# Kernel tuning notes

Hardware: AMD Instinct MI355X
Metric: run time of the kernel (lower is better)

Reference implementation:

```python
import jax, jax.numpy as jnp
import numpy as np

PAD = 4
MAX_DISP = 4


def setup_inputs() -> dict:
    key = jax.random.key(0)
    k1, k2 = jax.random.split(key)
    in1 = jax.random.normal(k1, (8, 256, 128, 128), dtype=jnp.float32)
    in2 = jax.random.normal(k2, (8, 256, 128, 128), dtype=jnp.float32)
    return {"in1": in1, "in2": in2}


def reference(in1, in2):
    # in1, in2: [B, C, H, W]
    H, W = in1.shape[2], in1.shape[3]
    in2_pad = jnp.pad(in2, ((0, 0), (0, 0), (PAD, PAD), (PAD, PAD)))
    D = 2 * MAX_DISP + 1  # 9 displacements per axis -> 81 output channels
    outs = []
    # torch.meshgrid('ij') + zip(offsetx, offsety): dy is the outer (slow) index,
    # dx the inner (fast) index.
    for dy in range(D):
        for dx in range(D):
            # mean over channel dim of elementwise product with shifted window
            corr = jnp.mean(in1 * in2_pad[:, :, dy:dy + H, dx:dx + W],
                            axis=1, keepdims=True)  # [B,1,H,W]
            outs.append(corr)
    return jnp.concatenate(outs, axis=1)  # [B, D*D, H, W]
```

## Files before the change

### kernel.cpp

```cpp
#include <hip/hip_runtime.h>


#define B_   8
#define C_   256
#define H_   128
#define W_   128
#define ND   9
#define TY   16
#define TW   16
#define CS   (H_ * W_)
#define NST  16
#define SB2  9216
#define S1OFF 73728
#define FOFF  106496
#define FAOFF 143360
#define LDS_TOTAL 159744

typedef short v8s __attribute__((ext_vector_type(8)));
typedef float v4f __attribute__((ext_vector_type(4)));

__device__ __forceinline__ unsigned short f2bf(float f) {
    union { float f; unsigned u; } v; v.f = f;
    return (unsigned short)((v.u + 0x7FFFu + ((v.u >> 16) & 1u)) >> 16);
}

__device__ __forceinline__ void dma16(const float* g, void* lds) {
    __builtin_amdgcn_global_load_lds(
        (const __attribute__((address_space(1))) void*)g,
        (__attribute__((address_space(3))) void*)lds, 16, 0, 0);
}

#define FENCE()     asm volatile("" ::: "memory")
#define WAITK_BAR() do {                                                          \
        if (w < 4) asm volatile("s_waitcnt vmcnt(7)\n\ts_barrier" ::: "memory");  \
        else       asm volatile("s_waitcnt vmcnt(6)\n\ts_barrier" ::: "memory");  \
    } while (0)
#define WAITV0_BAR() asm volatile("s_waitcnt vmcnt(0)\n\ts_barrier" ::: "memory")
#define LGKM0_BAR()  asm volatile("s_waitcnt lgkmcnt(0)\n\ts_barrier" ::: "memory")
#define LGKM0()      asm volatile("s_waitcnt lgkmcnt(0)" ::: "memory")

__global__ __launch_bounds__(512, 2)
void corr_mfma_kernel(const float* __restrict__ in1,
                      const float* __restrict__ in2,
                      float* __restrict__ out) {
    extern __shared__ __align__(16) char ldsbase[];
    float* S2 = (float*)ldsbase;
    float* S1 = (float*)(ldsbase + S1OFF);
    short* F  = (short*)(ldsbase + FOFF);
    short* FA = (short*)(ldsbase + FAOFF);
    float* EP = (float*)ldsbase;

    const int tid  = threadIdx.x;
    const int lane = tid & 63;
    const int w    = tid >> 6;

    const int lin = blockIdx.x;
    const int b   = lin & 7;
    const int idx = lin >> 3;
    const int x0  = (idx & 7) * TW;
    const int y0  = (idx >> 3) * TY;

    const int i_px = lane & 15;
    const int kb   = lane >> 4;

    const float* dsrc[5];
    int ddst[5];
    #pragma unroll
    for (int t = 0; t < 5; ++t) {
        if (w >= 4 && t >= 4) { dsrc[t] = in2; ddst[t] = 0; continue; }
        const int q   = (w < 4) ? (w * 5 + t) : (20 + (w - 4) * 4 + t);
        const int g   = q * 64 + lane;
        const int ccl = g / 144;
        const int rem = g % 144;
        const int r   = rem / 6;
        const int jg  = rem % 6;
        int gy = y0 - 4 + r;
        int gx = x0 - 4 + jg * 4;
        gy = gy < 0 ? 0 : (gy > H_ - 1 ? H_ - 1 : gy);
        gx = gx < 0 ? 0 : (gx > W_ - 4 ? W_ - 4 : gx);
        dsrc[t] = in2 + ((long)(b * C_) + ccl) * CS + gy * W_ + gx;
        ddst[t] = q * 1024;
    }
    const float* d1src[2];
    int d1dst[2];
    #pragma unroll
    for (int t = 0; t < 2; ++t) {
        const int q   = w * 2 + t;
        const int g   = q * 64 + lane;
        const int ch  = g >> 6;
        const int rem = g & 63;
        const int r   = rem >> 2;
        const int xg  = rem & 3;
        d1src[t] = in1 + ((long)(b * C_) + ch) * CS + (y0 + r) * W_ + x0 + xg * 4;
        d1dst[t] = q * 1024;
    }

    int rem_i[3], kbl_i[3];
    bool cval[3];
    #pragma unroll
    for (int it = 0; it < 3; ++it) {
        const int s2  = (tid + it * 512) % 1152;
        kbl_i[it] = s2 / 576;
        rem_i[it] = s2 % 576;
        const int r = rem_i[it] / 24, j = rem_i[it] % 24;
        cval[it] = ((unsigned)(y0 - 4 + r) < (unsigned)H_) &&
                   ((unsigned)(x0 - 4 + j) < (unsigned)W_);
    }
    const int r1  = tid >> 5;
    const int px1 = (tid >> 1) & 15;
    const int kb1 = tid & 1;

    v4f acc0[2][ND];
    v4f acc1[2][5];
    #pragma unroll
    for (int rw = 0; rw < 2; ++rw) {
        #pragma unroll
        for (int d = 0; d < ND; ++d) acc0[rw][d] = (v4f)0.0f;
        #pragma unroll
        for (int p = 0; p < 5; ++p)  acc1[rw][p] = (v4f)0.0f;
    }

#define ISSUE_G(s_) do {                                                      \
        const long so = (long)(s_) * 16 * CS;                                 \
        char* sb2 = (char*)S2 + ((s_) & 1) * 36864;                           \
        _Pragma("unroll")                                                     \
        for (int t = 0; t < 5; ++t)                                           \
            if (w < 4 || t < 4) dma16(dsrc[t] + so, sb2 + ddst[t]);           \
        char* sb1 = (char*)S1 + ((s_) & 1) * 16384;                           \
        _Pragma("unroll")                                                     \
        for (int t = 0; t < 2; ++t) dma16(d1src[t] + so, sb1 + d1dst[t]);     \
        FENCE();                                                              \
    } while (0)

#define CONVERT(s_) do {                                                      \
        const float* sb2 = S2 + ((s_) & 1) * SB2;                             \
        _Pragma("unroll")                                                     \
        for (int it = 0; it < 3; ++it) {                                      \
            if (it < 2 || tid < 128) {                                        \
                v8s pk;                                                       \
                _Pragma("unroll")                                             \
                for (int e = 0; e < 8; ++e)                                   \
                    pk[e] = (short)f2bf(sb2[kbl_i[it] * 4608 + rem_i[it] + e * 576]); \
                if (!cval[it]) pk = (v8s)0;                                   \
                const int kb32 = ((s_) & 1) * 2 + kbl_i[it];                  \
                *(v8s*)&F[kb32 * 4608 + (rem_i[it] << 3)] = pk;               \
            }                                                                 \
        }                                                                     \
        const float* sb1 = S1 + ((s_) & 1) * 4096;                            \
        v8s pa;                                                               \
        _Pragma("unroll")                                                     \
        for (int e = 0; e < 8; ++e)                                           \
            pa[e] = (short)f2bf(sb1[(kb1 * 8 + e) * 256 + r1 * 16 + px1]);    \
        *(v8s*)&FA[r1 * 512 + px1 * 32 + ((s_) & 1) * 16 + kb1 * 8] = pa;     \
    } while (0)

    ISSUE_G(0);
    ISSUE_G(1);
    WAITK_BAR();
    CONVERT(0);
    LGKM0_BAR();

    #pragma unroll
    for (int s = 0; s < NST; ++s) {
        if (s + 2 < NST) ISSUE_G(s + 2);

        if (s & 1) {
            const v8s af0 = *(const v8s*)&FA[(2 * w + 0) * 512 + i_px * 32 + kb * 8];
            const v8s af1 = *(const v8s*)&FA[(2 * w + 1) * 512 + i_px * 32 + kb * 8];
            #pragma unroll
            for (int u = 0; u < 10; ++u) {
                const int rj = (2 * w + u) * 24 + i_px;
                const v8s f = *(const v8s*)&F[kb * 4608 + (rj << 3)];
                if (u < 9)
                    acc0[0][u] = __builtin_amdgcn_mfma_f32_16x16x32_bf16(
                        af0, f, acc0[0][u], 0, 0, 0);
                if (u > 0)
                    acc0[1][u - 1] = __builtin_amdgcn_mfma_f32_16x16x32_bf16(
                        af1, f, acc0[1][u - 1], 0, 0, 0);
            }
            const int hi = i_px >> 3, j1 = 16 + (i_px & 7);
            #pragma unroll
            for (int u = 0; u < 10; ++u) {
                int r = 2 * w + hi + u;
                if (r > 23) r = 23;
                const int rj = r * 24 + j1;
                const v8s f = *(const v8s*)&F[kb * 4608 + (rj << 3)];
                if ((u & 1) == 0)
                    acc1[0][u >> 1] = __builtin_amdgcn_mfma_f32_16x16x32_bf16(
                        af0, f, acc1[0][u >> 1], 0, 0, 0);
                else
                    acc1[1][u >> 1] = __builtin_amdgcn_mfma_f32_16x16x32_bf16(
                        af1, f, acc1[1][u >> 1], 0, 0, 0);
            }
        }

        if (s + 2 < NST)       { WAITK_BAR(); }
        else if (s == NST - 2) { WAITV0_BAR(); }

        if (s < NST - 1) {
            CONVERT(s + 1);
            LGKM0_BAR();
        }
    }

    float* epw = EP + w * 384;
    const int g4 = lane >> 4;
    #pragma unroll
    for (int rw = 0; rw < 2; ++rw) {
        const int orow = y0 + 2 * w + rw;
        #pragma unroll
        for (int dy = 0; dy < ND; ++dy) {
            #pragma unroll
            for (int q = 0; q < 4; ++q)
                epw[(g4 * 4 + q) * 24 + i_px] = acc0[rw][dy][q];
            if ((i_px >> 3) == (dy & 1)) {
                #pragma unroll
                for (int q = 0; q < 4; ++q)
                    epw[(g4 * 4 + q) * 24 + 16 + (i_px & 7)] = acc1[rw][dy >> 1][q];
            }
            LGKM0();
            #pragma unroll
            for (int rep = 0; rep < 3; ++rep) {
                const int dx = g4 + rep * 4;
                if (dx < 9) {
                    const float v = epw[i_px * 24 + i_px + dx] * (1.0f / 256.0f);
                    out[(((long)b * 81 + dy * 9 + dx) * H_ + orow) * W_ + x0 + i_px] = v;
                }
            }
            LGKM0();
        }
    }
#undef ISSUE_G
#undef CONVERT
}

extern "C" void kernel_launch(void* const* d_in, const int* in_sizes, int n_in,
                              void* d_out, int out_size, void* d_ws, size_t ws_size,
                              hipStream_t stream) {
    const float* in1 = (const float*)d_in[0];
    const float* in2 = (const float*)d_in[1];
    float* outp      = (float*)d_out;
    (void)hipFuncSetAttribute((const void*)corr_mfma_kernel,
                              hipFuncAttributeMaxDynamicSharedMemorySize,
                              LDS_TOTAL);
    corr_mfma_kernel<<<512, 512, LDS_TOTAL, stream>>>(in1, in2, outp);
}
```

Measured before the change: 90.26 us.

## Widen tile to 32 columns with 1024-thread blocks and register-loaded in1 fragments

Doubles the output tile width to 16x32 and runs 256 blocks of 1024 threads (16 waves, one row each), which cuts the redundant halo traffic for in2 per output pixel. in1 is no longer staged through LDS. Each lane loads its A-fragment straight from global memory into registers a chunk ahead and converts it to bf16 in place. The in2 pipeline now streams 8 channels per stage into a four-deep bf16 ring, and the MFMAs run once per 32 channels. The trade-off is one block per CU with fewer blocks in flight, a hand-tuned vmcnt schedule, and strided uncoalesced-ish in1 loads.

```diff
diff --git a/kernel.cpp b/kernel.cpp
--- a/kernel.cpp
+++ b/kernel.cpp
@@ -7,14 +7,11 @@
 #define W_   128
 #define ND   9
 #define TY   16
-#define TW   16
+#define TW   32
 #define CS   (H_ * W_)
-#define NST  16
-#define SB2  9216
-#define S1OFF 73728
-#define FOFF  106496
-#define FAOFF 143360
-#define LDS_TOTAL 159744
+#define SB2F 7680
+#define FOFFB 61440
+#define LDS_TOTAL 122880
 
 typedef short v8s __attribute__((ext_vector_type(8)));
 typedef float v4f __attribute__((ext_vector_type(4)));
@@ -30,24 +27,26 @@
         (__attribute__((address_space(3))) void*)lds, 16, 0, 0);
 }
 
-#define FENCE()     asm volatile("" ::: "memory")
+#define FENCE()      asm volatile("" ::: "memory")
 #define WAITK_BAR() do {                                                          \
-        if (w < 4) asm volatile("s_waitcnt vmcnt(7)\n\ts_barrier" ::: "memory");  \
-        else       asm volatile("s_waitcnt vmcnt(6)\n\ts_barrier" ::: "memory");  \
+        if (w < 14) asm volatile("s_waitcnt vmcnt(2)\n\ts_barrier" ::: "memory"); \
+        else        asm volatile("s_waitcnt vmcnt(1)\n\ts_barrier" ::: "memory"); \
+    } while (0)
+#define WAITKA_BAR() do {                                                          \
+        if (w < 14) asm volatile("s_waitcnt vmcnt(18)\n\ts_barrier" ::: "memory"); \
+        else        asm volatile("s_waitcnt vmcnt(17)\n\ts_barrier" ::: "memory"); \
     } while (0)
 #define WAITV0_BAR() asm volatile("s_waitcnt vmcnt(0)\n\ts_barrier" ::: "memory")
 #define LGKM0_BAR()  asm volatile("s_waitcnt lgkmcnt(0)\n\ts_barrier" ::: "memory")
 #define LGKM0()      asm volatile("s_waitcnt lgkmcnt(0)" ::: "memory")
 
-__global__ __launch_bounds__(512, 2)
+__global__ __launch_bounds__(1024, 1)
 void corr_mfma_kernel(const float* __restrict__ in1,
                       const float* __restrict__ in2,
                       float* __restrict__ out) {
     extern __shared__ __align__(16) char ldsbase[];
     float* S2 = (float*)ldsbase;
-    float* S1 = (float*)(ldsbase + S1OFF);
-    short* F  = (short*)(ldsbase + FOFF);
-    short* FA = (short*)(ldsbase + FAOFF);
+    short* F  = (short*)(ldsbase + FOFFB);
     float* EP = (float*)ldsbase;
 
     const int tid  = threadIdx.x;
@@ -57,166 +56,151 @@
     const int lin = blockIdx.x;
     const int b   = lin & 7;
     const int idx = lin >> 3;
-    const int x0  = (idx & 7) * TW;
-    const int y0  = (idx >> 3) * TY;
+    const int x0  = (idx & 3) * TW;
+    const int y0  = (idx >> 2) * TY;
 
     const int i_px = lane & 15;
     const int kb   = lane >> 4;
 
-    const float* dsrc[5];
-    int ddst[5];
+    const float* dsrc[2];
+    int ddst[2];
     #pragma unroll
-    for (int t = 0; t < 5; ++t) {
-        if (w >= 4 && t >= 4) { dsrc[t] = in2; ddst[t] = 0; continue; }
-        const int q   = (w < 4) ? (w * 5 + t) : (20 + (w - 4) * 4 + t);
+    for (int t = 0; t < 2; ++t) {
+        if (t == 1 && w >= 14) { dsrc[t] = in2; ddst[t] = 0; continue; }
+        const int q   = (w < 14) ? (w * 2 + t) : (28 + (w - 14));
         const int g   = q * 64 + lane;
-        const int ccl = g / 144;
-        const int rem = g % 144;
-        const int r   = rem / 6;
-        const int jg  = rem % 6;
+        const int ch  = g / 240;
+        const int rem = g % 240;
+        const int r   = rem / 10;
+        const int jg  = rem % 10;
         int gy = y0 - 4 + r;
         int gx = x0 - 4 + jg * 4;
         gy = gy < 0 ? 0 : (gy > H_ - 1 ? H_ - 1 : gy);
         gx = gx < 0 ? 0 : (gx > W_ - 4 ? W_ - 4 : gx);
-        dsrc[t] = in2 + ((long)(b * C_) + ccl) * CS + gy * W_ + gx;
+        dsrc[t] = in2 + ((long)(b * C_) + ch) * CS + gy * W_ + gx;
         ddst[t] = q * 1024;
     }
-    const float* d1src[2];
-    int d1dst[2];
-    #pragma unroll
-    for (int t = 0; t < 2; ++t) {
-        const int q   = w * 2 + t;
-        const int g   = q * 64 + lane;
-        const int ch  = g >> 6;
-        const int rem = g & 63;
-        const int r   = rem >> 2;
-        const int xg  = rem & 3;
-        d1src[t] = in1 + ((long)(b * C_) + ch) * CS + (y0 + r) * W_ + x0 + xg * 4;
-        d1dst[t] = q * 1024;
-    }
-
-    int rem_i[3], kbl_i[3];
-    bool cval[3];
-    #pragma unroll
-    for (int it = 0; it < 3; ++it) {
-        const int s2  = (tid + it * 512) % 1152;
-        kbl_i[it] = s2 / 576;
-        rem_i[it] = s2 % 576;
-        const int r = rem_i[it] / 24, j = rem_i[it] % 24;
-        cval[it] = ((unsigned)(y0 - 4 + r) < (unsigned)H_) &&
-                   ((unsigned)(x0 - 4 + j) < (unsigned)W_);
-    }
-    const int r1  = tid >> 5;
-    const int px1 = (tid >> 1) & 15;
-    const int kb1 = tid & 1;
+
+    const float* pA =
+        in1 + ((long)b * C_ + kb * 8) * CS + (long)(y0 + w) * W_ + x0 + i_px;
+
+    const bool cact = (w < 15);
+    const int  crr  = tid / 40, cjj = tid % 40;
+    const bool cval = cact && ((unsigned)(y0 - 4 + crr) < (unsigned)H_) &&
+                              ((unsigned)(x0 - 4 + cjj) < (unsigned)W_);
 
     v4f acc0[2][ND];
     v4f acc1[2][5];
     #pragma unroll
-    for (int rw = 0; rw < 2; ++rw) {
+    for (int t = 0; t < 2; ++t) {
         #pragma unroll
-        for (int d = 0; d < ND; ++d) acc0[rw][d] = (v4f)0.0f;
+        for (int d = 0; d < ND; ++d) acc0[t][d] = (v4f)0.0f;
         #pragma unroll
-        for (int p = 0; p < 5; ++p)  acc1[rw][p] = (v4f)0.0f;
+        for (int p = 0; p < 5; ++p)  acc1[t][p] = (v4f)0.0f;
     }
+    float bufA[16], bufB[16];
+    v8s afA[2], afB[2];
 
 #define ISSUE_G(s_) do {                                                      \
-        const long so = (long)(s_) * 16 * CS;                                 \
-        char* sb2 = (char*)S2 + ((s_) & 1) * 36864;                           \
+        const long so = (long)(s_) * 8 * CS;                                  \
+        char* dst = (char*)S2 + ((s_) & 1) * 30720;                           \
+        dma16(dsrc[0] + so, dst + ddst[0]);                                   \
+        if (w < 14) dma16(dsrc[1] + so, dst + ddst[1]);                       \
+        FENCE();                                                              \
+    } while (0)
+
+#define ISSUE_A(cn_, buf_) do {                                               \
         _Pragma("unroll")                                                     \
-        for (int t = 0; t < 5; ++t)                                           \
-            if (w < 4 || t < 4) dma16(dsrc[t] + so, sb2 + ddst[t]);           \
-        char* sb1 = (char*)S1 + ((s_) & 1) * 16384;                           \
+        for (int t = 0; t < 2; ++t)                                           \
+            _Pragma("unroll")                                                 \
+            for (int e = 0; e < 8; ++e)                                       \
+                buf_[t * 8 + e] = pA[((long)(cn_) * 32 + e) * CS + t * 16];   \
+        FENCE();                                                              \
+    } while (0)
+
+#define AFRAG(buf_, af_) do {                                                 \
         _Pragma("unroll")                                                     \
-        for (int t = 0; t < 2; ++t) dma16(d1src[t] + so, sb1 + d1dst[t]);     \
-        FENCE();                                                              \
+        for (int t = 0; t < 2; ++t)                                           \
+            _Pragma("unroll")                                                 \
+            for (int e = 0; e < 8; ++e)                                       \
+                af_[t][e] = (short)f2bf(buf_[t * 8 + e]);                     \
     } while (0)
 
 #define CONVERT(s_) do {                                                      \
-        const float* sb2 = S2 + ((s_) & 1) * SB2;                             \
+        if (cact) {                                                           \
+            const float* sh = S2 + ((s_) & 1) * SB2F;                         \
+            v8s pk;                                                           \
+            _Pragma("unroll")                                                 \
+            for (int e = 0; e < 8; ++e)                                       \
+                pk[e] = (short)f2bf(sh[e * 960 + tid]);                       \
+            if (!cval) pk = (v8s)0;                                           \
+            *(v8s*)&F[(((s_) % 4) * 960 + tid) * 8] = pk;                     \
+        }                                                                     \
+    } while (0)
+
+#define MFMA_C(af_) do {                                                      \
         _Pragma("unroll")                                                     \
-        for (int it = 0; it < 3; ++it) {                                      \
-            if (it < 2 || tid < 128) {                                        \
-                v8s pk;                                                       \
-                _Pragma("unroll")                                             \
-                for (int e = 0; e < 8; ++e)                                   \
-                    pk[e] = (short)f2bf(sb2[kbl_i[it] * 4608 + rem_i[it] + e * 576]); \
-                if (!cval[it]) pk = (v8s)0;                                   \
-                const int kb32 = ((s_) & 1) * 2 + kbl_i[it];                  \
-                *(v8s*)&F[kb32 * 4608 + (rem_i[it] << 3)] = pk;               \
+        for (int t = 0; t < 2; ++t) {                                         \
+            _Pragma("unroll")                                                 \
+            for (int dy = 0; dy < ND; ++dy) {                                 \
+                const v8s f = *(const v8s*)&F[(kb * 960 + (w + dy) * 40 + t * 16 + i_px) * 8]; \
+                acc0[t][dy] = __builtin_amdgcn_mfma_f32_16x16x32_bf16(        \
+                    af_[t], f, acc0[t][dy], 0, 0, 0);                         \
+            }                                                                 \
+            const int hi = i_px >> 3, j1 = t * 16 + 16 + (i_px & 7);          \
+            _Pragma("unroll")                                                 \
+            for (int P = 0; P < 5; ++P) {                                     \
+                int r = w + 2 * P + hi;                                       \
+                if (r > 23) r = 23;            \
+                const v8s f = *(const v8s*)&F[(kb * 960 + r * 40 + j1) * 8];  \
+                acc1[t][P] = __builtin_amdgcn_mfma_f32_16x16x32_bf16(         \
+                    af_[t], f, acc1[t][P], 0, 0, 0);                          \
             }                                                                 \
         }                                                                     \
-        const float* sb1 = S1 + ((s_) & 1) * 4096;                            \
-        v8s pa;                                                               \
-        _Pragma("unroll")                                                     \
-        for (int e = 0; e < 8; ++e)                                           \
-            pa[e] = (short)f2bf(sb1[(kb1 * 8 + e) * 256 + r1 * 16 + px1]);    \
-        *(v8s*)&FA[r1 * 512 + px1 * 32 + ((s_) & 1) * 16 + kb1 * 8] = pa;     \
-    } while (0)
-
+    } while (0)
+
+#define CHUNK(c_, afc_, afn_, bufn_) do {                                     \
+        ISSUE_G(4*(c_)+2); WAITK_BAR();  CONVERT(4*(c_)+1); LGKM0_BAR();      \
+        ISSUE_G(4*(c_)+3); WAITK_BAR();  CONVERT(4*(c_)+2); LGKM0_BAR();      \
+        ISSUE_A((c_)+1, bufn_);                                               \
+        ISSUE_G(4*(c_)+4); WAITKA_BAR(); CONVERT(4*(c_)+3); LGKM0_BAR();      \
+        ISSUE_G(4*(c_)+5); MFMA_C(afc_); WAITK_BAR();                         \
+        CONVERT(4*(c_)+4); AFRAG(bufn_, afn_); LGKM0_BAR();                   \
+    } while (0)
+
+    ISSUE_A(0, bufA);
     ISSUE_G(0);
     ISSUE_G(1);
     WAITK_BAR();
+    AFRAG(bufA, afA);
     CONVERT(0);
     LGKM0_BAR();
 
-    #pragma unroll
-    for (int s = 0; s < NST; ++s) {
-        if (s + 2 < NST) ISSUE_G(s + 2);
-
-        if (s & 1) {
-            const v8s af0 = *(const v8s*)&FA[(2 * w + 0) * 512 + i_px * 32 + kb * 8];
-            const v8s af1 = *(const v8s*)&FA[(2 * w + 1) * 512 + i_px * 32 + kb * 8];
-            #pragma unroll
-            for (int u = 0; u < 10; ++u) {
-                const int rj = (2 * w + u) * 24 + i_px;
-                const v8s f = *(const v8s*)&F[kb * 4608 + (rj << 3)];
-                if (u < 9)
-                    acc0[0][u] = __builtin_amdgcn_mfma_f32_16x16x32_bf16(
-                        af0, f, acc0[0][u], 0, 0, 0);
-                if (u > 0)
-                    acc0[1][u - 1] = __builtin_amdgcn_mfma_f32_16x16x32_bf16(
-                        af1, f, acc0[1][u - 1], 0, 0, 0);
-            }
-            const int hi = i_px >> 3, j1 = 16 + (i_px & 7);
-            #pragma unroll
-            for (int u = 0; u < 10; ++u) {
-                int r = 2 * w + hi + u;
-                if (r > 23) r = 23;
-                const int rj = r * 24 + j1;
-                const v8s f = *(const v8s*)&F[kb * 4608 + (rj << 3)];
-                if ((u & 1) == 0)
-                    acc1[0][u >> 1] = __builtin_amdgcn_mfma_f32_16x16x32_bf16(
-                        af0, f, acc1[0][u >> 1], 0, 0, 0);
-                else
-                    acc1[1][u >> 1] = __builtin_amdgcn_mfma_f32_16x16x32_bf16(
-                        af1, f, acc1[1][u >> 1], 0, 0, 0);
-            }
-        }
-
-        if (s + 2 < NST)       { WAITK_BAR(); }
-        else if (s == NST - 2) { WAITV0_BAR(); }
-
-        if (s < NST - 1) {
-            CONVERT(s + 1);
-            LGKM0_BAR();
-        }
-    }
+    CHUNK(0, afA, afB, bufB);
+    CHUNK(1, afB, afA, bufA);
+    CHUNK(2, afA, afB, bufB);
+    CHUNK(3, afB, afA, bufA);
+    CHUNK(4, afA, afB, bufB);
+    CHUNK(5, afB, afA, bufA);
+    CHUNK(6, afA, afB, bufB);
+    ISSUE_G(30); WAITK_BAR();  CONVERT(29); LGKM0_BAR();
+    ISSUE_G(31); WAITK_BAR();  CONVERT(30); LGKM0_BAR();
+    WAITV0_BAR();              CONVERT(31); LGKM0_BAR();
+    MFMA_C(afB);
 
     float* epw = EP + w * 384;
     const int g4 = lane >> 4;
     #pragma unroll
-    for (int rw = 0; rw < 2; ++rw) {
-        const int orow = y0 + 2 * w + rw;
+    for (int t = 0; t < 2; ++t) {
         #pragma unroll
         for (int dy = 0; dy < ND; ++dy) {
             #pragma unroll
             for (int q = 0; q < 4; ++q)
-                epw[(g4 * 4 + q) * 24 + i_px] = acc0[rw][dy][q];
+                epw[(g4 * 4 + q) * 24 + i_px] = acc0[t][dy][q];
             if ((i_px >> 3) == (dy & 1)) {
                 #pragma unroll
                 for (int q = 0; q < 4; ++q)
-                    epw[(g4 * 4 + q) * 24 + 16 + (i_px & 7)] = acc1[rw][dy >> 1][q];
+                    epw[(g4 * 4 + q) * 24 + 16 + (i_px & 7)] = acc1[t][dy >> 1][q];
             }
             LGKM0();
             #pragma unroll
@@ -224,14 +208,18 @@
                 const int dx = g4 + rep * 4;
                 if (dx < 9) {
                     const float v = epw[i_px * 24 + i_px + dx] * (1.0f / 256.0f);
-                    out[(((long)b * 81 + dy * 9 + dx) * H_ + orow) * W_ + x0 + i_px] = v;
+                    out[(((long)b * 81 + dy * 9 + dx) * CS) + (y0 + w) * W_ + x0 + t * 16 + i_px] = v;
                 }
             }
             LGKM0();
         }
     }
 #undef ISSUE_G
+#undef ISSUE_A
+#undef AFRAG
 #undef CONVERT
+#undef MFMA_C
+#undef CHUNK
 }
 
 extern "C" void kernel_launch(void* const* d_in, const int* in_sizes, int n_in,
@@ -243,5 +231,5 @@
     (void)hipFuncSetAttribute((const void*)corr_mfma_kernel,
                               hipFuncAttributeMaxDynamicSharedMemorySize,
                               LDS_TOTAL);
-    corr_mfma_kernel<<<512, 512, LDS_TOTAL, stream>>>(in1, in2, outp);
-}
+    corr_mfma_kernel<<<256, 1024, LDS_TOTAL, stream>>>(in1, in2, outp);
+}
```

After: 258.2 us. +186.1%, slower.

## Double block size to 1024 threads with one output row per wave

Applied to the files above, without the earlier changes.

The kernel now launches 16 waves per block instead of 8, and each wave computes one output row instead of two. The in2/in1 DMA and conversion work is redistributed across the extra waves, and the vmcnt thresholds are adjusted to match the smaller per-wave load count. This halves the accumulator registers per thread and adds more waves to hide latency. In exchange it gives up reuse of the shared F fragments across two rows, which raises the total LDS fragment reads, and the 1024-thread barriers become more expensive.

```diff
diff --git a/kernel.cpp b/kernel.cpp
--- a/kernel.cpp
+++ b/kernel.cpp
@@ -32,14 +32,14 @@
 
 #define FENCE()     asm volatile("" ::: "memory")
 #define WAITK_BAR() do {                                                          \
-        if (w < 4) asm volatile("s_waitcnt vmcnt(7)\n\ts_barrier" ::: "memory");  \
-        else       asm volatile("s_waitcnt vmcnt(6)\n\ts_barrier" ::: "memory");  \
+        if (w < 4) asm volatile("s_waitcnt vmcnt(4)\n\ts_barrier" ::: "memory");  \
+        else       asm volatile("s_waitcnt vmcnt(3)\n\ts_barrier" ::: "memory");  \
     } while (0)
 #define WAITV0_BAR() asm volatile("s_waitcnt vmcnt(0)\n\ts_barrier" ::: "memory")
 #define LGKM0_BAR()  asm volatile("s_waitcnt lgkmcnt(0)\n\ts_barrier" ::: "memory")
 #define LGKM0()      asm volatile("s_waitcnt lgkmcnt(0)" ::: "memory")
 
-__global__ __launch_bounds__(512, 2)
+__global__ __launch_bounds__(1024, 4)
 void corr_mfma_kernel(const float* __restrict__ in1,
                       const float* __restrict__ in2,
                       float* __restrict__ out) {
@@ -63,12 +63,12 @@
     const int i_px = lane & 15;
     const int kb   = lane >> 4;
 
-    const float* dsrc[5];
-    int ddst[5];
-    #pragma unroll
-    for (int t = 0; t < 5; ++t) {
-        if (w >= 4 && t >= 4) { dsrc[t] = in2; ddst[t] = 0; continue; }
-        const int q   = (w < 4) ? (w * 5 + t) : (20 + (w - 4) * 4 + t);
+    const float* dsrc[3];
+    int ddst[3];
+    #pragma unroll
+    for (int t = 0; t < 3; ++t) {
+        if (w >= 4 && t >= 2) { dsrc[t] = in2; ddst[t] = 0; continue; }
+        const int q   = (w < 4) ? (w * 3 + t) : (12 + (w - 4) * 2 + t);
         const int g   = q * 64 + lane;
         const int ccl = g / 144;
         const int rem = g % 144;
@@ -81,62 +81,55 @@
         dsrc[t] = in2 + ((long)(b * C_) + ccl) * CS + gy * W_ + gx;
         ddst[t] = q * 1024;
     }
-    const float* d1src[2];
-    int d1dst[2];
-    #pragma unroll
-    for (int t = 0; t < 2; ++t) {
-        const int q   = w * 2 + t;
-        const int g   = q * 64 + lane;
+    const float* d1src;
+    int d1dst;
+    {
+        const int g   = w * 64 + lane;
         const int ch  = g >> 6;
         const int rem = g & 63;
         const int r   = rem >> 2;
         const int xg  = rem & 3;
-        d1src[t] = in1 + ((long)(b * C_) + ch) * CS + (y0 + r) * W_ + x0 + xg * 4;
-        d1dst[t] = q * 1024;
-    }
-
-    int rem_i[3], kbl_i[3];
-    bool cval[3];
-    #pragma unroll
-    for (int it = 0; it < 3; ++it) {
-        const int s2  = (tid + it * 512) % 1152;
+        d1src = in1 + ((long)(b * C_) + ch) * CS + (y0 + r) * W_ + x0 + xg * 4;
+        d1dst = w * 1024;
+    }
+
+    int rem_i[2], kbl_i[2];
+    bool cval[2];
+    #pragma unroll
+    for (int it = 0; it < 2; ++it) {
+        const int s2 = tid + it * 1024;
         kbl_i[it] = s2 / 576;
         rem_i[it] = s2 % 576;
         const int r = rem_i[it] / 24, j = rem_i[it] % 24;
         cval[it] = ((unsigned)(y0 - 4 + r) < (unsigned)H_) &&
                    ((unsigned)(x0 - 4 + j) < (unsigned)W_);
     }
-    const int r1  = tid >> 5;
+    const int r1  = (tid >> 5) & 15;
     const int px1 = (tid >> 1) & 15;
     const int kb1 = tid & 1;
 
-    v4f acc0[2][ND];
-    v4f acc1[2][5];
-    #pragma unroll
-    for (int rw = 0; rw < 2; ++rw) {
-        #pragma unroll
-        for (int d = 0; d < ND; ++d) acc0[rw][d] = (v4f)0.0f;
-        #pragma unroll
-        for (int p = 0; p < 5; ++p)  acc1[rw][p] = (v4f)0.0f;
-    }
+    v4f acc0[ND];
+    v4f acc1[5];
+    #pragma unroll
+    for (int d = 0; d < ND; ++d) acc0[d] = (v4f)0.0f;
+    #pragma unroll
+    for (int p = 0; p < 5; ++p)  acc1[p] = (v4f)0.0f;
 
 #define ISSUE_G(s_) do {                                                      \
         const long so = (long)(s_) * 16 * CS;                                 \
         char* sb2 = (char*)S2 + ((s_) & 1) * 36864;                           \
         _Pragma("unroll")                                                     \
-        for (int t = 0; t < 5; ++t)                                           \
-            if (w < 4 || t < 4) dma16(dsrc[t] + so, sb2 + ddst[t]);           \
-        char* sb1 = (char*)S1 + ((s_) & 1) * 16384;                           \
-        _Pragma("unroll")                                                     \
-        for (int t = 0; t < 2; ++t) dma16(d1src[t] + so, sb1 + d1dst[t]);     \
+        for (int t = 0; t < 3; ++t)                                           \
+            if (w < 4 || t < 2) dma16(dsrc[t] + so, sb2 + ddst[t]);           \
+        dma16(d1src + so, (char*)ldsbase + S1OFF + ((s_) & 1) * 16384 + d1dst); \
         FENCE();                                                              \
     } while (0)
 
 #define CONVERT(s_) do {                                                      \
         const float* sb2 = S2 + ((s_) & 1) * SB2;                             \
         _Pragma("unroll")                                                     \
-        for (int it = 0; it < 3; ++it) {                                      \
-            if (it < 2 || tid < 128) {                                        \
+        for (int it = 0; it < 2; ++it) {                                      \
+            if (it < 1 || tid < 128) {                                        \
                 v8s pk;                                                       \
                 _Pragma("unroll")                                             \
                 for (int e = 0; e < 8; ++e)                                   \
@@ -146,12 +139,14 @@
                 *(v8s*)&F[kb32 * 4608 + (rem_i[it] << 3)] = pk;               \
             }                                                                 \
         }                                                                     \
-        const float* sb1 = S1 + ((s_) & 1) * 4096;                            \
-        v8s pa;                                                               \
-        _Pragma("unroll")                                                     \
-        for (int e = 0; e < 8; ++e)                                           \
-            pa[e] = (short)f2bf(sb1[(kb1 * 8 + e) * 256 + r1 * 16 + px1]);    \
-        *(v8s*)&FA[r1 * 512 + px1 * 32 + ((s_) & 1) * 16 + kb1 * 8] = pa;     \
+        if (tid < 512) {                                                      \
+            const float* sb1 = S1 + ((s_) & 1) * 4096;                        \
+            v8s pa;                                                           \
+            _Pragma("unroll")                                                 \
+            for (int e = 0; e < 8; ++e)                                       \
+                pa[e] = (short)f2bf(sb1[(kb1 * 8 + e) * 256 + r1 * 16 + px1]); \
+            *(v8s*)&FA[r1 * 512 + px1 * 32 + ((s_) & 1) * 16 + kb1 * 8] = pa; \
+        }                                                                     \
     } while (0)
 
     ISSUE_G(0);
@@ -165,32 +160,23 @@
         if (s + 2 < NST) ISSUE_G(s + 2);
 
         if (s & 1) {
-            const v8s af0 = *(const v8s*)&FA[(2 * w + 0) * 512 + i_px * 32 + kb * 8];
-            const v8s af1 = *(const v8s*)&FA[(2 * w + 1) * 512 + i_px * 32 + kb * 8];
+            const v8s af = *(const v8s*)&FA[w * 512 + i_px * 32 + kb * 8];
             #pragma unroll
-            for (int u = 0; u < 10; ++u) {
-                const int rj = (2 * w + u) * 24 + i_px;
+            for (int dy = 0; dy < ND; ++dy) {
+                const int rj = (w + dy) * 24 + i_px;
                 const v8s f = *(const v8s*)&F[kb * 4608 + (rj << 3)];
-                if (u < 9)
-                    acc0[0][u] = __builtin_amdgcn_mfma_f32_16x16x32_bf16(
-                        af0, f, acc0[0][u], 0, 0, 0);
-                if (u > 0)
-                    acc0[1][u - 1] = __builtin_amdgcn_mfma_f32_16x16x32_bf16(
-                        af1, f, acc0[1][u - 1], 0, 0, 0);
+                acc0[dy] = __builtin_amdgcn_mfma_f32_16x16x32_bf16(
+                    af, f, acc0[dy], 0, 0, 0);
             }
             const int hi = i_px >> 3, j1 = 16 + (i_px & 7);
             #pragma unroll
-            for (int u = 0; u < 10; ++u) {
-                int r = 2 * w + hi + u;
+            for (int P = 0; P < 5; ++P) {
+                int r = w + 2 * P + hi;
                 if (r > 23) r = 23;
                 const int rj = r * 24 + j1;
                 const v8s f = *(const v8s*)&F[kb * 4608 + (rj << 3)];
-                if ((u & 1) == 0)
-                    acc1[0][u >> 1] = __builtin_amdgcn_mfma_f32_16x16x32_bf16(
-                        af0, f, acc1[0][u >> 1], 0, 0, 0);
-                else
-                    acc1[1][u >> 1] = __builtin_amdgcn_mfma_f32_16x16x32_bf16(
-                        af1, f, acc1[1][u >> 1], 0, 0, 0);
+                acc1[P] = __builtin_amdgcn_mfma_f32_16x16x32_bf16(
+                    af, f, acc1[P], 0, 0, 0);
             }
         }
 
@@ -206,32 +192,26 @@
     float* epw = EP + w * 384;
     const int g4 = lane >> 4;
     #pragma unroll
-    for (int rw = 0; rw < 2; ++rw) {
-        const int orow = y0 + 2 * w + rw;
+    for (int dy = 0; dy < ND; ++dy) {
         #pragma unroll
-        for (int dy = 0; dy < ND; ++dy) {
+        for (int q = 0; q < 4; ++q)
+            epw[(g4 * 4 + q) * 24 + i_px] = acc0[dy][q];
+        if ((i_px >> 3) == (dy & 1)) {
             #pragma unroll
             for (int q = 0; q < 4; ++q)
-                epw[(g4 * 4 + q) * 24 + i_px] = acc0[rw][dy][q];
-            if ((i_px >> 3) == (dy & 1)) {
-                #pragma unroll
-                for (int q = 0; q < 4; ++q)
-                    epw[(g4 * 4 + q) * 24 + 16 + (i_px & 7)] = acc1[rw][dy >> 1][q];
+                epw[(g4 * 4 + q) * 24 + 16 + (i_px & 7)] = acc1[dy >> 1][q];
+        }
+        LGKM0();
+        #pragma unroll
+        for (int rep = 0; rep < 3; ++rep) {
+            const int dx = g4 + rep * 4;
+            if (dx < 9) {
+                const float v = epw[i_px * 24 + i_px + dx] * (1.0f / 256.0f);
+                out[((long)b * 81 + dy * 9 + dx) * CS + (y0 + w) * W_ + x0 + i_px] = v;
             }
-            LGKM0();
-            #pragma unroll
-            for (int rep = 0; rep < 3; ++rep) {
-                const int dx = g4 + rep * 4;
-                if (dx < 9) {
-                    const float v = epw[i_px * 24 + i_px + dx] * (1.0f / 256.0f);
-                    out[(((long)b * 81 + dy * 9 + dx) * H_ + orow) * W_ + x0 + i_px] = v;
-                }
-            }
-            LGKM0();
-        }
-    }
-#undef ISSUE_G
-#undef CONVERT
+        }
+        LGKM0();
+    }
 }
 
 extern "C" void kernel_launch(void* const* d_in, const int* in_sizes, int n_in,
@@ -243,5 +223,5 @@
     (void)hipFuncSetAttribute((const void*)corr_mfma_kernel,
                               hipFuncAttributeMaxDynamicSharedMemorySize,
                               LDS_TOTAL);
-    corr_mfma_kernel<<<512, 512, LDS_TOTAL, stream>>>(in1, in2, outp);
-}
+    corr_mfma_kernel<<<512, 1024, LDS_TOTAL, stream>>>(in1, in2, outp);
+}
```

After: 88.95 us. No clear change (-1.5%).
